# Performance work log

Measured on AMD Instinct MI355X. Metric: run time of the kernel, lower is better.

Reference implementation:

```python
import jax, jax.numpy as jnp
import numpy as np

# Quantum circuits here are products of single-qubit gates (no entanglement),
# so PauliZ expectations have closed forms:
#   attention head (RX(x) then trainable RX(theta)):  <Z> = cos(x + theta)
#   ffn qlayer    (RX(x) then trainable RY(phi)):     <Z> = cos(x) * cos(phi)

LN_EPS = 1e-5

def layernorm(x, g, b):
    mu = jnp.mean(x, axis=-1, keepdims=True)
    var = jnp.mean((x - mu) ** 2, axis=-1, keepdims=True)
    return (x - mu) * jax.lax.rsqrt(var + LN_EPS) * g + b

def sinusoidal_pe(S, E):
    pos = jnp.arange(S, dtype=jnp.float32)[:, None]
    div = jnp.exp(jnp.arange(0, E, 2, dtype=jnp.float32) * (-np.log(10000.0) / E))
    pe = jnp.zeros((S, E), dtype=jnp.float32)
    pe = pe.at[:, 0::2].set(jnp.sin(pos * div))
    pe = pe.at[:, 1::2].set(jnp.cos(pos * div))
    return pe

def setup_inputs() -> dict:
    key = jax.random.key(0)
    V, E, H, L, F, C, NQ = 32000, 512, 128, 6, 2048, 10, 4
    B, S = 8, 2048
    ks = jax.random.split(key, 16)
    s = 0.02
    return {
        "tokens": jax.random.randint(ks[0], (B, S), 0, V, dtype=jnp.int32),
        "emb": jax.random.normal(ks[1], (V, E), jnp.float32) * s,
        "theta_attn": jax.random.normal(ks[2], (L, H, NQ), jnp.float32),
        "combine_W": jax.random.normal(ks[3], (L, E, E), jnp.float32) * s,
        "combine_b": jnp.zeros((L, E), jnp.float32),
        "ln1_g": jnp.ones((L, E), jnp.float32),
        "ln1_b": jnp.zeros((L, E), jnp.float32),
        "phi_ffn": jax.random.normal(ks[4], (L, NQ), jnp.float32),
        "lin1_W": jax.random.normal(ks[5], (L, F, NQ), jnp.float32) * s,
        "lin1_b": jnp.zeros((L, F), jnp.float32),
        "lin2_W": jax.random.normal(ks[6], (L, E, F), jnp.float32) * s,
        "lin2_b": jnp.zeros((L, E), jnp.float32),
        "ln2_g": jnp.ones((L, E), jnp.float32),
        "ln2_b": jnp.zeros((L, E), jnp.float32),
        "cls_W": jax.random.normal(ks[7], (C, E), jnp.float32) * s,
        "cls_b": jnp.zeros((C,), jnp.float32),
    }

def reference(tokens, emb, theta_attn, combine_W, combine_b, ln1_g, ln1_b,
              phi_ffn, lin1_W, lin1_b, lin2_W, lin2_b, ln2_g, ln2_b,
              cls_W, cls_b):
    B, S = tokens.shape
    E = emb.shape[1]
    L, H, NQ = theta_attn.shape
    dk = E // H  # == NQ by construction
    x = emb[tokens] + sinusoidal_pe(S, E)[None]  # (B,S,E)
    nqf = phi_ffn.shape[1]
    for l in range(L):
        # quantum multi-head attention: per-token per-head <Z> = cos(x + theta)
        heads = x.reshape(B, S, H, dk)
        attn_q = jnp.cos(heads + theta_attn[l][None, None]).reshape(B, S, E)
        attn = jnp.einsum('bse,fe->bsf', attn_q, combine_W[l]) + combine_b[l]
        x = layernorm(x + attn, ln1_g[l], ln1_b[l])
        # quantum FFN: <Z> = cos(x_i) * cos(phi_i) on first nqf features
        z = jnp.cos(x[..., :nqf]) * jnp.cos(phi_ffn[l])  # (B,S,nqf)
        h = jax.nn.relu(jnp.einsum('bsq,fq->bsf', z, lin1_W[l]) + lin1_b[l])
        ffn = jnp.einsum('bsf,ef->bse', h, lin2_W[l]) + lin2_b[l]
        x = layernorm(x + ffn, ln2_g[l], ln2_b[l])
    pooled = jnp.mean(x, axis=1)  # (B,E) mean-pool over sequence
    return pooled @ cls_W.T + cls_b  # (B,C)
```

## Files before the change

### kernel.cpp

```cpp
#include <hip/hip_runtime.h>
#include <hip/hip_bf16.h>
#include <math.h>

#define LN_EPS 1e-5f

constexpr int Bb = 8, Ss = 2048, Ee = 512, Ll = 6, Ff = 2048, Cc = 10;
constexpr int Nn = Bb * Ss;

typedef __attribute__((ext_vector_type(8))) short short8v;
typedef __attribute__((ext_vector_type(4))) float f32x4;

__device__ __forceinline__ unsigned short f2bf(float f) {
    unsigned int b = __float_as_uint(f);
    b += 0x7FFFu + ((b >> 16) & 1u);
    return (unsigned short)(b >> 16);
}

__device__ __forceinline__ float fastcos(float x) {
    float r = x * 0.15915494309189535f;
    r = __builtin_amdgcn_fractf(r);
    return __builtin_amdgcn_cosf(r);
}

__device__ __forceinline__ void gload16(const void* g, void* lds) {
    __builtin_amdgcn_global_load_lds(
        (__attribute__((address_space(1))) void*)(g),
        (__attribute__((address_space(3))) void*)(lds),
        16, 0, 0);
}

__global__ void pe_kernel(float* __restrict__ pe) {
    int p = blockIdx.x * blockDim.x + threadIdx.x;
    int total = Ss * (Ee / 2);
    if (p >= total) return;
    int s = p / (Ee / 2);
    int i = p % (Ee / 2);
    float div = expf(float(2 * i) * (-logf(10000.0f) / float(Ee)));
    float ang = float(s) * div;
    pe[s * Ee + 2 * i]     = sinf(ang);
    pe[s * Ee + 2 * i + 1] = cosf(ang);
}

__global__ void embed_kernel(const int* __restrict__ tokens,
                             const float* __restrict__ emb,
                             const float* __restrict__ pe,
                             const float* __restrict__ theta0,
                             float* __restrict__ x,
                             unsigned short* __restrict__ acos) {
    int idx = blockIdx.x * blockDim.x + threadIdx.x;
    int total = Nn * Ee / 4;
    if (idx >= total) return;
    int n  = idx / (Ee / 4);
    int e4 = idx % (Ee / 4);
    int tok = tokens[n];
    int s = n % Ss;
    f32x4 a = *(const f32x4*)(emb + (size_t)tok * Ee + e4 * 4);
    f32x4 p = *(const f32x4*)(pe + (size_t)s * Ee + e4 * 4);
    f32x4 o = a + p;
    *(f32x4*)(x + (size_t)n * Ee + e4 * 4) = o;
    f32x4 t = *(const f32x4*)(theta0 + e4 * 4);
    ushort4 c;
    c.x = f2bf(fastcos(o.x + t.x));
    c.y = f2bf(fastcos(o.y + t.y));
    c.z = f2bf(fastcos(o.z + t.z));
    c.w = f2bf(fastcos(o.w + t.w));
    *(ushort4*)(acos + (size_t)n * Ee + e4 * 4) = c;
}

__global__ void cvt_bf16(const float* __restrict__ in,
                         unsigned short* __restrict__ out, int n4) {
    int i = blockIdx.x * blockDim.x + threadIdx.x;
    if (i >= n4) return;
    f32x4 v = *(const f32x4*)(in + (size_t)i * 4);
    ushort4 o;
    o.x = f2bf(v.x); o.y = f2bf(v.y); o.z = f2bf(v.z); o.w = f2bf(v.w);
    *(ushort4*)(out + (size_t)i * 4) = o;
}

__global__ __launch_bounds__(256) void h_kernel(const float* __restrict__ z,
                                                const float* __restrict__ W1,
                                                const float* __restrict__ b1,
                                                unsigned short* __restrict__ H) {
    __shared__ unsigned short hls[8 * Ff];
    const int t  = threadIdx.x;
    const int m0 = blockIdx.x * 8;
    f32x4 zr[8];
#pragma unroll
    for (int r = 0; r < 8; ++r)
        zr[r] = *(const f32x4*)(z + (size_t)(m0 + r) * 4);
#pragma unroll
    for (int j = 0; j < 8; ++j) {
        const int f = t + 256 * j;
        f32x4 w = *(const f32x4*)(W1 + (size_t)f * 4);
        float bb = b1[f];
#pragma unroll
        for (int r = 0; r < 8; ++r) {
            float v = zr[r].x * w.x + zr[r].y * w.y + zr[r].z * w.z +
                      zr[r].w * w.w + bb;
            hls[r * Ff + f] = f2bf(fmaxf(v, 0.f));
        }
    }
    __syncthreads();
#pragma unroll
    for (int j = 0; j < 8; ++j) {
        const int idx = (j * 256 + t) * 8;
        *(short8v*)(H + (size_t)m0 * Ff + idx) = *(const short8v*)(&hls[idx]);
    }
}

__global__ __launch_bounds__(512, 4) void gemm_bf16(
    const unsigned short* __restrict__ A,
    const unsigned short* __restrict__ Wb,
    const float* __restrict__ bias,
    const float* __restrict__ xres,
    float* __restrict__ Cout,
    int K) {
    __shared__ unsigned short As[2][128 * 64];
    __shared__ unsigned short Bs[2][128 * 64];
    const int tid  = threadIdx.x;
    const int lane = tid & 63;
    const int wid  = tid >> 6;
    const int wr   = wid >> 2;
    const int wc   = wid & 3;
    const int wg   = blockIdx.x;
    const int sw   = (wg & 7) * 64 + (wg >> 3);
    const int row0 = (sw >> 2) * 128;
    const int col0 = (sw & 3) * 128;
    const int srow   = lane >> 3;
    const int pchunk = lane & 7;

    f32x4 acc[4][2];
#pragma unroll
    for (int m = 0; m < 4; m++)
#pragma unroll
        for (int n = 0; n < 2; n++) acc[m][n] = {0.f, 0.f, 0.f, 0.f};

    const int NT = K >> 6;

    auto STAGE = [&](int buf, int k0) {
#pragma unroll
        for (int i = 0; i < 2; ++i) {
            const int s   = wid * 2 + i;
            const int row = s * 8 + srow;
            const int lc  = pchunk ^ (row & 7);
            gload16(A  + (size_t)(row0 + row) * K + k0 + lc * 8, &As[buf][s * 512]);
        }
#pragma unroll
        for (int i = 0; i < 2; ++i) {
            const int s   = wid * 2 + i;
            const int row = s * 8 + srow;
            const int lc  = pchunk ^ (row & 7);
            gload16(Wb + (size_t)(col0 + row) * K + k0 + lc * 8, &Bs[buf][s * 512]);
        }
    };

    STAGE(0, 0);
    if (NT > 1) STAGE(1, 64);
    for (int kt = 0; kt < NT; ++kt) {
        const int b = kt & 1;
        if (kt + 1 < NT) {
            asm volatile("s_waitcnt vmcnt(4)" ::: "memory");
        } else {
            asm volatile("s_waitcnt vmcnt(0)" ::: "memory");
        }
        __builtin_amdgcn_s_barrier();
        asm volatile("" ::: "memory");
        short8v aF[2][4], bF[2][2];
#pragma unroll
        for (int ks = 0; ks < 2; ks++) {
            const int k8 = ks * 4 + (lane >> 4);
#pragma unroll
            for (int m = 0; m < 4; m++) {
                const int row = wr * 64 + m * 16 + (lane & 15);
                aF[ks][m] = *(const short8v*)(&As[b][row * 64 + ((k8 ^ (row & 7)) * 8)]);
            }
#pragma unroll
            for (int n = 0; n < 2; n++) {
                const int row = wc * 32 + n * 16 + (lane & 15);
                bF[ks][n] = *(const short8v*)(&Bs[b][row * 64 + ((k8 ^ (row & 7)) * 8)]);
            }
        }
        asm volatile("s_waitcnt lgkmcnt(0)" ::: "memory");
        __builtin_amdgcn_s_barrier();
        asm volatile("" ::: "memory");
        if (kt + 2 < NT) STAGE(b, (kt + 2) << 6);
#pragma unroll
        for (int ks = 0; ks < 2; ks++)
#pragma unroll
            for (int m = 0; m < 4; m++)
#pragma unroll
                for (int n = 0; n < 2; n++)
                    acc[m][n] = __builtin_amdgcn_mfma_f32_16x16x32_bf16(
                        aF[ks][m], bF[ks][n], acc[m][n], 0, 0, 0);
    }

#pragma unroll
    for (int m = 0; m < 4; m++) {
#pragma unroll
        for (int n = 0; n < 2; n++) {
            int colg = col0 + wc * 32 + n * 16 + (lane & 15);
            float bv = bias[colg];
#pragma unroll
            for (int j = 0; j < 4; j++) {
                int rowg = row0 + wr * 64 + m * 16 + ((lane >> 4) * 4) + j;
                size_t off = (size_t)rowg * 512 + colg;
                Cout[off] = acc[m][n][j] + bv + xres[off];
            }
        }
    }
}

__global__ __launch_bounds__(256) void ln_fused(
    const float* __restrict__ tmp, float* __restrict__ x,
    const float* __restrict__ g, const float* __restrict__ b,
    const float* __restrict__ phi, float* __restrict__ z,
    const float* __restrict__ theta, unsigned short* __restrict__ acos) {
    const int row  = blockIdx.x * 4 + (threadIdx.x >> 6);
    const int lane = threadIdx.x & 63;
    const float* tr = tmp + (size_t)row * Ee;
    f32x4 v0 = *(const f32x4*)(tr + lane * 4);
    f32x4 v1 = *(const f32x4*)(tr + 256 + lane * 4);
    float s = v0.x + v0.y + v0.z + v0.w + v1.x + v1.y + v1.z + v1.w;
#pragma unroll
    for (int o = 32; o; o >>= 1) s += __shfl_xor(s, o);
    float mu = s * (1.f / 512.f);
    f32x4 d0 = {v0.x - mu, v0.y - mu, v0.z - mu, v0.w - mu};
    f32x4 d1 = {v1.x - mu, v1.y - mu, v1.z - mu, v1.w - mu};
    float q = d0.x * d0.x + d0.y * d0.y + d0.z * d0.z + d0.w * d0.w +
              d1.x * d1.x + d1.y * d1.y + d1.z * d1.z + d1.w * d1.w;
#pragma unroll
    for (int o = 32; o; o >>= 1) q += __shfl_xor(q, o);
    float rs = rsqrtf(q * (1.f / 512.f) + LN_EPS);
    f32x4 g0 = *(const f32x4*)(g + lane * 4);
    f32x4 b0 = *(const f32x4*)(b + lane * 4);
    f32x4 g1 = *(const f32x4*)(g + 256 + lane * 4);
    f32x4 b1v = *(const f32x4*)(b + 256 + lane * 4);
    f32x4 o0 = {d0.x * rs * g0.x + b0.x, d0.y * rs * g0.y + b0.y,
                d0.z * rs * g0.z + b0.z, d0.w * rs * g0.w + b0.w};
    f32x4 o1 = {d1.x * rs * g1.x + b1v.x, d1.y * rs * g1.y + b1v.y,
                d1.z * rs * g1.z + b1v.z, d1.w * rs * g1.w + b1v.w};
    *(f32x4*)(x + (size_t)row * Ee + lane * 4) = o0;
    *(f32x4*)(x + (size_t)row * Ee + 256 + lane * 4) = o1;
    if (z != nullptr && lane == 0) {
        z[(size_t)row * 4 + 0] = fastcos(o0.x) * fastcos(phi[0]);
        z[(size_t)row * 4 + 1] = fastcos(o0.y) * fastcos(phi[1]);
        z[(size_t)row * 4 + 2] = fastcos(o0.z) * fastcos(phi[2]);
        z[(size_t)row * 4 + 3] = fastcos(o0.w) * fastcos(phi[3]);
    }
    if (acos != nullptr) {
        f32x4 t0 = *(const f32x4*)(theta + lane * 4);
        f32x4 t1 = *(const f32x4*)(theta + 256 + lane * 4);
        ushort4 c0, c1;
        c0.x = f2bf(fastcos(o0.x + t0.x));
        c0.y = f2bf(fastcos(o0.y + t0.y));
        c0.z = f2bf(fastcos(o0.z + t0.z));
        c0.w = f2bf(fastcos(o0.w + t0.w));
        c1.x = f2bf(fastcos(o1.x + t1.x));
        c1.y = f2bf(fastcos(o1.y + t1.y));
        c1.z = f2bf(fastcos(o1.z + t1.z));
        c1.w = f2bf(fastcos(o1.w + t1.w));
        *(ushort4*)(acos + (size_t)row * Ee + lane * 4) = c0;
        *(ushort4*)(acos + (size_t)row * Ee + 256 + lane * 4) = c1;
    }
}

__global__ __launch_bounds__(256) void pool_part(const float* __restrict__ x,
                                                 float* __restrict__ part) {
    int bidx = blockIdx.x, ch = blockIdx.y;
    int t = threadIdx.x;
    float s0 = 0.f, s1 = 0.f;
    for (int s = 0; s < 64; ++s) {
        const float* row = x + ((size_t)bidx * Ss + ch * 64 + s) * Ee;
        s0 += row[t];
        s1 += row[t + 256];
    }
    float* pr = part + ((size_t)(bidx * 32 + ch)) * Ee;
    pr[t] = s0;
    pr[t + 256] = s1;
}

__global__ __launch_bounds__(256) void cls_kernel(const float* __restrict__ part,
                                                  const float* __restrict__ clsW,
                                                  const float* __restrict__ clsb,
                                                  float* __restrict__ out) {
    int bidx = blockIdx.x;
    int t = threadIdx.x;
    float p0 = 0.f, p1 = 0.f;
    for (int ch = 0; ch < 32; ++ch) {
        const float* pr = part + ((size_t)(bidx * 32 + ch)) * Ee;
        p0 += pr[t];
        p1 += pr[t + 256];
    }
    p0 *= (1.f / float(Ss));
    p1 *= (1.f / float(Ss));
    __shared__ float red[256];
    for (int c = 0; c < Cc; ++c) {
        red[t] = p0 * clsW[(size_t)c * Ee + t] + p1 * clsW[(size_t)c * Ee + t + 256];
        __syncthreads();
        for (int s2 = 128; s2 > 0; s2 >>= 1) {
            if (t < s2) red[t] += red[t + s2];
            __syncthreads();
        }
        if (t == 0) out[bidx * Cc + c] = red[0] + clsb[c];
        __syncthreads();
    }
}

extern "C" void kernel_launch(void* const* d_in, const int* in_sizes, int n_in,
                              void* d_out, int out_size, void* d_ws, size_t ws_size,
                              hipStream_t stream) {
    const int*   tokens     = (const int*)d_in[0];
    const float* emb        = (const float*)d_in[1];
    const float* theta_attn = (const float*)d_in[2];
    const float* combine_W  = (const float*)d_in[3];
    const float* combine_b  = (const float*)d_in[4];
    const float* ln1_g      = (const float*)d_in[5];
    const float* ln1_b      = (const float*)d_in[6];
    const float* phi_ffn    = (const float*)d_in[7];
    const float* lin1_W     = (const float*)d_in[8];
    const float* lin1_b     = (const float*)d_in[9];
    const float* lin2_W     = (const float*)d_in[10];
    const float* lin2_b     = (const float*)d_in[11];
    const float* ln2_g      = (const float*)d_in[12];
    const float* ln2_b      = (const float*)d_in[13];
    const float* cls_W      = (const float*)d_in[14];
    const float* cls_b      = (const float*)d_in[15];
    float* out = (float*)d_out;

    float* x    = (float*)d_ws;
    float* tmp  = x + (size_t)Nn * Ee;
    float* z    = tmp + (size_t)Nn * Ee;
    float* part = z + (size_t)Nn * 4;
    unsigned short* Wcb  = (unsigned short*)(part + (size_t)Bb * 32 * Ee);
    unsigned short* W2b  = Wcb + (size_t)Ll * Ee * Ee;
    unsigned short* acos = W2b + (size_t)Ll * Ee * Ff;
    unsigned short* H    = acos + (size_t)Nn * Ee;
    float* pe = (float*)H;

    {
        int total = Ss * (Ee / 2);
        pe_kernel<<<(total + 255) / 256, 256, 0, stream>>>(pe);
    }
    {
        int total = Nn * Ee / 4;
        embed_kernel<<<(total + 255) / 256, 256, 0, stream>>>(
            tokens, emb, pe, theta_attn, x, acos);
    }
    {
        int n4c = Ll * Ee * Ee / 4;
        cvt_bf16<<<(n4c + 255) / 256, 256, 0, stream>>>(combine_W, Wcb, n4c);
        int n42 = Ll * Ee * Ff / 4;
        cvt_bf16<<<(n42 + 255) / 256, 256, 0, stream>>>(lin2_W, W2b, n42);
    }

    const int ngemm = (Nn / 128) * (Ee / 128);
    for (int l = 0; l < Ll; l++) {
        const unsigned short* cWl = Wcb + (size_t)l * Ee * Ee;
        const float* cbl  = combine_b + (size_t)l * Ee;
        const float* g1   = ln1_g + (size_t)l * Ee;
        const float* b1n  = ln1_b + (size_t)l * Ee;
        const float* phil = phi_ffn + (size_t)l * 4;
        const float* w1l  = lin1_W + (size_t)l * Ff * 4;
        const float* b1l  = lin1_b + (size_t)l * Ff;
        const unsigned short* w2l = W2b + (size_t)l * Ee * Ff;
        const float* b2l  = lin2_b + (size_t)l * Ee;
        const float* g2   = ln2_g + (size_t)l * Ee;
        const float* b2n  = ln2_b + (size_t)l * Ee;
        const float* thn  = (l + 1 < Ll) ? theta_attn + (size_t)(l + 1) * Ee : nullptr;
        unsigned short* acn = (l + 1 < Ll) ? acos : nullptr;

        gemm_bf16<<<ngemm, 512, 0, stream>>>(acos, cWl, cbl, x, tmp, Ee);
        ln_fused<<<Nn / 4, 256, 0, stream>>>(tmp, x, g1, b1n, phil, z,
                                             nullptr, nullptr);
        h_kernel<<<Nn / 8, 256, 0, stream>>>(z, w1l, b1l, H);
        gemm_bf16<<<ngemm, 512, 0, stream>>>(H, w2l, b2l, x, tmp, Ff);
        ln_fused<<<Nn / 4, 256, 0, stream>>>(tmp, x, g2, b2n, nullptr, nullptr,
                                             thn, acn);
    }

    pool_part<<<dim3(Bb, 32), 256, 0, stream>>>(x, part);
    cls_kernel<<<Bb, 256, 0, stream>>>(part, cls_W, cls_b, out);
}
```

Baseline: 638.8 us.

## Store GEMM residual output in bf16 and process two rows per LayerNorm wave

The GEMM epilogue now writes the pre-LayerNorm sum (acc + bias + residual) as bf16 instead of fp32, which halves the intermediate buffer traffic between the GEMM and the LayerNorm kernel. The LayerNorm kernel reads bf16, has each wave handle two rows, launches half as many blocks, and hoists the cos(phi) terms out of the per-element loop. The cost is reduced precision before LayerNorm, where the residual stream itself is rounded to bf16 every layer, so error can build up across the six layers.

Result: slower. 659.9 us (+3.3%).

```diff
diff --git a/kernel.cpp b/kernel.cpp
--- a/kernel.cpp
+++ b/kernel.cpp
@@ -14,6 +14,10 @@
     unsigned int b = __float_as_uint(f);
     b += 0x7FFFu + ((b >> 16) & 1u);
     return (unsigned short)(b >> 16);
+}
+
+__device__ __forceinline__ float bf2f(unsigned short u) {
+    return __uint_as_float((unsigned int)u << 16);
 }
 
 __device__ __forceinline__ float fastcos(float x) {
@@ -113,7 +117,7 @@
     const unsigned short* __restrict__ Wb,
     const float* __restrict__ bias,
     const float* __restrict__ xres,
-    float* __restrict__ Cout,
+    unsigned short* __restrict__ Coutb,
     int K) {
     __shared__ unsigned short As[2][128 * 64];
     __shared__ unsigned short Bs[2][128 * 64];
@@ -204,63 +208,111 @@
             for (int j = 0; j < 4; j++) {
                 int rowg = row0 + wr * 64 + m * 16 + ((lane >> 4) * 4) + j;
                 size_t off = (size_t)rowg * 512 + colg;
-                Cout[off] = acc[m][n][j] + bv + xres[off];
+                Coutb[off] = f2bf(acc[m][n][j] + bv + xres[off]);
             }
         }
     }
 }
 
 __global__ __launch_bounds__(256) void ln_fused(
-    const float* __restrict__ tmp, float* __restrict__ x,
+    const unsigned short* __restrict__ tmp, float* __restrict__ x,
     const float* __restrict__ g, const float* __restrict__ b,
     const float* __restrict__ phi, float* __restrict__ z,
     const float* __restrict__ theta, unsigned short* __restrict__ acos) {
-    const int row  = blockIdx.x * 4 + (threadIdx.x >> 6);
+    const int wv   = threadIdx.x >> 6;
     const int lane = threadIdx.x & 63;
-    const float* tr = tmp + (size_t)row * Ee;
-    f32x4 v0 = *(const f32x4*)(tr + lane * 4);
-    f32x4 v1 = *(const f32x4*)(tr + 256 + lane * 4);
-    float s = v0.x + v0.y + v0.z + v0.w + v1.x + v1.y + v1.z + v1.w;
-#pragma unroll
-    for (int o = 32; o; o >>= 1) s += __shfl_xor(s, o);
-    float mu = s * (1.f / 512.f);
-    f32x4 d0 = {v0.x - mu, v0.y - mu, v0.z - mu, v0.w - mu};
-    f32x4 d1 = {v1.x - mu, v1.y - mu, v1.z - mu, v1.w - mu};
-    float q = d0.x * d0.x + d0.y * d0.y + d0.z * d0.z + d0.w * d0.w +
-              d1.x * d1.x + d1.y * d1.y + d1.z * d1.z + d1.w * d1.w;
-#pragma unroll
-    for (int o = 32; o; o >>= 1) q += __shfl_xor(q, o);
-    float rs = rsqrtf(q * (1.f / 512.f) + LN_EPS);
+    const int row0 = blockIdx.x * 8 + wv * 2;
+
     f32x4 g0 = *(const f32x4*)(g + lane * 4);
     f32x4 b0 = *(const f32x4*)(b + lane * 4);
     f32x4 g1 = *(const f32x4*)(g + 256 + lane * 4);
     f32x4 b1v = *(const f32x4*)(b + 256 + lane * 4);
-    f32x4 o0 = {d0.x * rs * g0.x + b0.x, d0.y * rs * g0.y + b0.y,
-                d0.z * rs * g0.z + b0.z, d0.w * rs * g0.w + b0.w};
-    f32x4 o1 = {d1.x * rs * g1.x + b1v.x, d1.y * rs * g1.y + b1v.y,
-                d1.z * rs * g1.z + b1v.z, d1.w * rs * g1.w + b1v.w};
-    *(f32x4*)(x + (size_t)row * Ee + lane * 4) = o0;
-    *(f32x4*)(x + (size_t)row * Ee + 256 + lane * 4) = o1;
+
+    f32x4 vA0, vA1, vB0, vB1;
+    {
+        const unsigned short* t0 = tmp + (size_t)row0 * Ee;
+        const unsigned short* t1 = tmp + (size_t)(row0 + 1) * Ee;
+        ushort4 a0 = *(const ushort4*)(t0 + lane * 4);
+        ushort4 a1 = *(const ushort4*)(t0 + 256 + lane * 4);
+        ushort4 c0 = *(const ushort4*)(t1 + lane * 4);
+        ushort4 c1 = *(const ushort4*)(t1 + 256 + lane * 4);
+        vA0 = {bf2f(a0.x), bf2f(a0.y), bf2f(a0.z), bf2f(a0.w)};
+        vA1 = {bf2f(a1.x), bf2f(a1.y), bf2f(a1.z), bf2f(a1.w)};
+        vB0 = {bf2f(c0.x), bf2f(c0.y), bf2f(c0.z), bf2f(c0.w)};
+        vB1 = {bf2f(c1.x), bf2f(c1.y), bf2f(c1.z), bf2f(c1.w)};
+    }
+    float s0 = vA0.x + vA0.y + vA0.z + vA0.w + vA1.x + vA1.y + vA1.z + vA1.w;
+    float s1 = vB0.x + vB0.y + vB0.z + vB0.w + vB1.x + vB1.y + vB1.z + vB1.w;
+#pragma unroll
+    for (int o = 32; o; o >>= 1) {
+        s0 += __shfl_xor(s0, o);
+        s1 += __shfl_xor(s1, o);
+    }
+    float mu0 = s0 * (1.f / 512.f), mu1 = s1 * (1.f / 512.f);
+    f32x4 dA0 = {vA0.x - mu0, vA0.y - mu0, vA0.z - mu0, vA0.w - mu0};
+    f32x4 dA1 = {vA1.x - mu0, vA1.y - mu0, vA1.z - mu0, vA1.w - mu0};
+    f32x4 dB0 = {vB0.x - mu1, vB0.y - mu1, vB0.z - mu1, vB0.w - mu1};
+    f32x4 dB1 = {vB1.x - mu1, vB1.y - mu1, vB1.z - mu1, vB1.w - mu1};
+    float q0 = dA0.x * dA0.x + dA0.y * dA0.y + dA0.z * dA0.z + dA0.w * dA0.w +
+               dA1.x * dA1.x + dA1.y * dA1.y + dA1.z * dA1.z + dA1.w * dA1.w;
+    float q1 = dB0.x * dB0.x + dB0.y * dB0.y + dB0.z * dB0.z + dB0.w * dB0.w +
+               dB1.x * dB1.x + dB1.y * dB1.y + dB1.z * dB1.z + dB1.w * dB1.w;
+#pragma unroll
+    for (int o = 32; o; o >>= 1) {
+        q0 += __shfl_xor(q0, o);
+        q1 += __shfl_xor(q1, o);
+    }
+    float rs0 = rsqrtf(q0 * (1.f / 512.f) + LN_EPS);
+    float rs1 = rsqrtf(q1 * (1.f / 512.f) + LN_EPS);
+
+    f32x4 oA0 = {dA0.x * rs0 * g0.x + b0.x, dA0.y * rs0 * g0.y + b0.y,
+                 dA0.z * rs0 * g0.z + b0.z, dA0.w * rs0 * g0.w + b0.w};
+    f32x4 oA1 = {dA1.x * rs0 * g1.x + b1v.x, dA1.y * rs0 * g1.y + b1v.y,
+                 dA1.z * rs0 * g1.z + b1v.z, dA1.w * rs0 * g1.w + b1v.w};
+    f32x4 oB0 = {dB0.x * rs1 * g0.x + b0.x, dB0.y * rs1 * g0.y + b0.y,
+                 dB0.z * rs1 * g0.z + b0.z, dB0.w * rs1 * g0.w + b0.w};
+    f32x4 oB1 = {dB1.x * rs1 * g1.x + b1v.x, dB1.y * rs1 * g1.y + b1v.y,
+                 dB1.z * rs1 * g1.z + b1v.z, dB1.w * rs1 * g1.w + b1v.w};
+    *(f32x4*)(x + (size_t)row0 * Ee + lane * 4) = oA0;
+    *(f32x4*)(x + (size_t)row0 * Ee + 256 + lane * 4) = oA1;
+    *(f32x4*)(x + (size_t)(row0 + 1) * Ee + lane * 4) = oB0;
+    *(f32x4*)(x + (size_t)(row0 + 1) * Ee + 256 + lane * 4) = oB1;
     if (z != nullptr && lane == 0) {
-        z[(size_t)row * 4 + 0] = fastcos(o0.x) * fastcos(phi[0]);
-        z[(size_t)row * 4 + 1] = fastcos(o0.y) * fastcos(phi[1]);
-        z[(size_t)row * 4 + 2] = fastcos(o0.z) * fastcos(phi[2]);
-        z[(size_t)row * 4 + 3] = fastcos(o0.w) * fastcos(phi[3]);
+        float c0p = fastcos(phi[0]), c1p = fastcos(phi[1]);
+        float c2p = fastcos(phi[2]), c3p = fastcos(phi[3]);
+        z[(size_t)row0 * 4 + 0] = fastcos(oA0.x) * c0p;
+        z[(size_t)row0 * 4 + 1] = fastcos(oA0.y) * c1p;
+        z[(size_t)row0 * 4 + 2] = fastcos(oA0.z) * c2p;
+        z[(size_t)row0 * 4 + 3] = fastcos(oA0.w) * c3p;
+        z[(size_t)(row0 + 1) * 4 + 0] = fastcos(oB0.x) * c0p;
+        z[(size_t)(row0 + 1) * 4 + 1] = fastcos(oB0.y) * c1p;
+        z[(size_t)(row0 + 1) * 4 + 2] = fastcos(oB0.z) * c2p;
+        z[(size_t)(row0 + 1) * 4 + 3] = fastcos(oB0.w) * c3p;
     }
     if (acos != nullptr) {
         f32x4 t0 = *(const f32x4*)(theta + lane * 4);
         f32x4 t1 = *(const f32x4*)(theta + 256 + lane * 4);
-        ushort4 c0, c1;
-        c0.x = f2bf(fastcos(o0.x + t0.x));
-        c0.y = f2bf(fastcos(o0.y + t0.y));
-        c0.z = f2bf(fastcos(o0.z + t0.z));
-        c0.w = f2bf(fastcos(o0.w + t0.w));
-        c1.x = f2bf(fastcos(o1.x + t1.x));
-        c1.y = f2bf(fastcos(o1.y + t1.y));
-        c1.z = f2bf(fastcos(o1.z + t1.z));
-        c1.w = f2bf(fastcos(o1.w + t1.w));
-        *(ushort4*)(acos + (size_t)row * Ee + lane * 4) = c0;
-        *(ushort4*)(acos + (size_t)row * Ee + 256 + lane * 4) = c1;
+        ushort4 cA0, cA1, cB0, cB1;
+        cA0.x = f2bf(fastcos(oA0.x + t0.x));
+        cA0.y = f2bf(fastcos(oA0.y + t0.y));
+        cA0.z = f2bf(fastcos(oA0.z + t0.z));
+        cA0.w = f2bf(fastcos(oA0.w + t0.w));
+        cA1.x = f2bf(fastcos(oA1.x + t1.x));
+        cA1.y = f2bf(fastcos(oA1.y + t1.y));
+        cA1.z = f2bf(fastcos(oA1.z + t1.z));
+        cA1.w = f2bf(fastcos(oA1.w + t1.w));
+        cB0.x = f2bf(fastcos(oB0.x + t0.x));
+        cB0.y = f2bf(fastcos(oB0.y + t0.y));
+        cB0.z = f2bf(fastcos(oB0.z + t0.z));
+        cB0.w = f2bf(fastcos(oB0.w + t0.w));
+        cB1.x = f2bf(fastcos(oB1.x + t1.x));
+        cB1.y = f2bf(fastcos(oB1.y + t1.y));
+        cB1.z = f2bf(fastcos(oB1.z + t1.z));
+        cB1.w = f2bf(fastcos(oB1.w + t1.w));
+        *(ushort4*)(acos + (size_t)row0 * Ee + lane * 4) = cA0;
+        *(ushort4*)(acos + (size_t)row0 * Ee + 256 + lane * 4) = cA1;
+        *(ushort4*)(acos + (size_t)(row0 + 1) * Ee + lane * 4) = cB0;
+        *(ushort4*)(acos + (size_t)(row0 + 1) * Ee + 256 + lane * 4) = cB1;
     }
 }
 
@@ -328,8 +380,8 @@
     float* out = (float*)d_out;
 
     float* x    = (float*)d_ws;
-    float* tmp  = x + (size_t)Nn * Ee;
-    float* z    = tmp + (size_t)Nn * Ee;
+    unsigned short* tmpb = (unsigned short*)(x + (size_t)Nn * Ee);
+    float* z    = (float*)(tmpb + (size_t)Nn * Ee);
     float* part = z + (size_t)Nn * 4;
     unsigned short* Wcb  = (unsigned short*)(part + (size_t)Bb * 32 * Ee);
     unsigned short* W2b  = Wcb + (size_t)Ll * Ee * Ee;
@@ -369,12 +421,12 @@
         const float* thn  = (l + 1 < Ll) ? theta_attn + (size_t)(l + 1) * Ee : nullptr;
         unsigned short* acn = (l + 1 < Ll) ? acos : nullptr;
 
-        gemm_bf16<<<ngemm, 512, 0, stream>>>(acos, cWl, cbl, x, tmp, Ee);
-        ln_fused<<<Nn / 4, 256, 0, stream>>>(tmp, x, g1, b1n, phil, z,
+        gemm_bf16<<<ngemm, 512, 0, stream>>>(acos, cWl, cbl, x, tmpb, Ee);
+        ln_fused<<<Nn / 8, 256, 0, stream>>>(tmpb, x, g1, b1n, phil, z,
                                              nullptr, nullptr);
         h_kernel<<<Nn / 8, 256, 0, stream>>>(z, w1l, b1l, H);
-        gemm_bf16<<<ngemm, 512, 0, stream>>>(H, w2l, b2l, x, tmp, Ff);
-        ln_fused<<<Nn / 4, 256, 0, stream>>>(tmp, x, g2, b2n, nullptr, nullptr,
+        gemm_bf16<<<ngemm, 512, 0, stream>>>(H, w2l, b2l, x, tmpb, Ff);
+        ln_fused<<<Nn / 8, 256, 0, stream>>>(tmpb, x, g2, b2n, nullptr, nullptr,
                                              thn, acn);
     }
 
```
